# Optimization experiments

Hardware: AMD Instinct MI355X
Metric: run time of the kernel (lower is better)

## Reference

```python
import jax, jax.numpy as jnp
import numpy as np

B, S, D_IN, D_OUT, N, R = 8, 4096, 1280, 1280, 4, 16


def setup_inputs() -> dict:
    key = jax.random.key(0)
    ks = jax.random.split(key, 7)
    x = jax.random.normal(ks[0], (B, S, D_IN), dtype=jnp.float32)
    W = jax.random.normal(ks[1], (D_OUT, D_IN), dtype=jnp.float32) * 0.02
    bias = jax.random.normal(ks[2], (D_OUT,), dtype=jnp.float32) * 0.02
    A = jax.random.normal(ks[3], (N, R, D_IN), dtype=jnp.float32) * 0.02
    Bw = jax.random.normal(ks[4], (N, D_OUT, R), dtype=jnp.float32) * 0.02
    scalings = jax.random.uniform(ks[5], (N,), dtype=jnp.float32)
    masks = jax.random.uniform(ks[6], (N, S), dtype=jnp.float32)
    # normalize masks to sum ~1 per position, per docstring
    masks = masks / jnp.sum(masks, axis=0, keepdims=True)
    return {"x": x, "W": W, "bias": bias, "A": A, "Bw": Bw,
            "scalings": scalings, "masks": masks}


def reference(x, W, bias, A, Bw, scalings, masks):
    # base linear: y = x @ W^T + b
    base = jnp.einsum('bsd,od->bso', x, W) + bias
    # batched LoRA branches: h = x @ A_i^T  (b,s,n,r)
    h = jnp.einsum('bsd,nrd->bsnr', x, A)
    # lora_out_i = h @ B_i^T  (b,s,n,o)
    lora = jnp.einsum('bsnr,nor->bsno', h, Bw)
    # weighted sum over subjects: scaling_i * mask_i(pos)
    lora_sum = jnp.einsum('bsno,n,ns->bso', lora, scalings, masks)
    return base + lora_sum
```

## Files before the change

### kernel.cpp

```cpp
#include <hip/hip_runtime.h>
#include <hip/hip_bf16.h>
#include <stdint.h>

#define S_LEN   4096
#define DIN     1280
#define DOUT    1280
#define N_LORA  4
#define R_LORA  16
#define M_TOT   32768
#define KC      (DIN + N_LORA*R_LORA)

typedef __attribute__((ext_vector_type(4))) float floatx4;
typedef __attribute__((ext_vector_type(8))) short shortx8;

static __device__ __forceinline__ unsigned short bf16_rne(float f) {
    union { float f; unsigned u; } v; v.f = f;
    unsigned u = v.u;
    u += 0x7fffu + ((u >> 16) & 1u);
    return (unsigned short)(u >> 16);
}

static __device__ __forceinline__ void async16(const unsigned short* g, unsigned short* l) {
    __builtin_amdgcn_global_load_lds(
        (const __attribute__((address_space(1))) unsigned int*)g,
        (__attribute__((address_space(3))) unsigned int*)l, 16, 0, 0);
}

static __device__ __forceinline__ uint4 cvt8(const float* src) {
    const float4* p = (const float4*)src;
    float4 a = p[0], b = p[1];
    uint4 o;
    o.x = (unsigned)bf16_rne(a.x) | ((unsigned)bf16_rne(a.y) << 16);
    o.y = (unsigned)bf16_rne(a.z) | ((unsigned)bf16_rne(a.w) << 16);
    o.z = (unsigned)bf16_rne(b.x) | ((unsigned)bf16_rne(b.y) << 16);
    o.w = (unsigned)bf16_rne(b.z) | ((unsigned)bf16_rne(b.w) << 16);
    return o;
}

__global__ __launch_bounds__(256) void k_convert_x(const float* __restrict__ x,
                                                   unsigned short* __restrict__ xg) {
    int i = blockIdx.x * 256 + threadIdx.x;
    int e = i * 8;
    int m = e / DIN;
    int k = e - m * DIN;
    uint4 o = cvt8(x + e);
    *(uint4*)(xg + m * KC + k) = o;
}

__global__ __launch_bounds__(256) void k_build_wcat(const float* __restrict__ W,
                                                    const float* __restrict__ Bw,
                                                    unsigned short* __restrict__ Wcat) {
    int i = blockIdx.x * 256 + threadIdx.x;
    int e = i * 8;
    int o = e / KC;
    int c = e - o * KC;
    const float* src;
    if (c < DIN) {
        src = W + o * DIN + c;
    } else {
        int j = c - DIN;
        int n = j >> 4, r = j & 15;
        src = Bw + (n * DOUT + o) * R_LORA + r;
    }
    *(uint4*)(Wcat + o * KC + c) = cvt8(src);
}

__global__ __launch_bounds__(256) void k_convert_a(const float* __restrict__ A,
                                                   unsigned short* __restrict__ Ab) {
    int i = blockIdx.x * 256 + threadIdx.x;
    int e = i * 8;
    *(uint4*)(Ab + e) = cvt8(A + e);
}

__global__ __launch_bounds__(256) void k_lora_g(const unsigned short* __restrict__ xg_in,
                                                const unsigned short* __restrict__ Ab,
                                                const float* __restrict__ scalings,
                                                const float* __restrict__ masks,
                                                unsigned short* __restrict__ xg_out) {
    __shared__ unsigned short Xs[64 * 32];
    __shared__ unsigned short As[64 * 32];
    int tid = threadIdx.x;
    int wave = tid >> 6, lane = tid & 63;
    int mi = lane & 15, kq = lane >> 4;
    int m0 = blockIdx.x * 64;

    int chunk = tid;
    int srow = chunk >> 2;
    int skc  = (chunk & 3) * 8;

    floatx4 acc[4] = {};

    for (int k0 = 0; k0 < DIN; k0 += 32) {
        async16(xg_in + (m0 + srow) * KC + k0 + skc, Xs + chunk * 8);
        async16(Ab + srow * DIN + k0 + skc,          As + chunk * 8);
        __syncthreads();
        shortx8 xf = *(const shortx8*)(Xs + (wave * 16 + mi) * 32 + kq * 8);
#pragma unroll
        for (int ct = 0; ct < 4; ++ct) {
            shortx8 af = *(const shortx8*)(As + (ct * 16 + mi) * 32 + kq * 8);
            acc[ct] = __builtin_amdgcn_mfma_f32_16x16x32_bf16(xf, af, acc[ct], 0, 0, 0);
        }
        __syncthreads();
    }

#pragma unroll
    for (int ct = 0; ct < 4; ++ct) {
        float sc = scalings[ct];
        int j = ct * 16 + mi;
#pragma unroll
        for (int reg = 0; reg < 4; ++reg) {
            int m = m0 + wave * 16 + kq * 4 + reg;
            int s = m & (S_LEN - 1);
            float wgt = sc * masks[ct * S_LEN + s];
            xg_out[m * KC + DIN + j] = bf16_rne(acc[ct][reg] * wgt);
        }
    }
}

__global__ __launch_bounds__(256) void k_main_gemm(const unsigned short* __restrict__ xg,
                                                   const unsigned short* __restrict__ Wcat,
                                                   const float* __restrict__ bias,
                                                   float* __restrict__ out) {
    __shared__ unsigned short As[128 * 32];
    __shared__ unsigned short Bs[128 * 32];
    int tid = threadIdx.x;
    int wave = tid >> 6, lane = tid & 63;
    int bx = blockIdx.x;
    int cb = bx % 10, rb = bx / 10;
    int m0 = rb * 128, n0 = cb * 128;
    int wr = wave >> 1, wc = wave & 1;
    int mi = lane & 15, kq = lane >> 4;

    int c0 = tid, c1 = tid + 256;
    int ar0 = c0 >> 2, ak0 = (c0 & 3) * 8;
    int ar1 = c1 >> 2, ak1 = (c1 & 3) * 8;

    floatx4 acc[4][4] = {};

    for (int k0 = 0; k0 < KC; k0 += 32) {
        async16(xg   + (m0 + ar0) * KC + k0 + ak0, As + c0 * 8);
        async16(xg   + (m0 + ar1) * KC + k0 + ak1, As + c1 * 8);
        async16(Wcat + (n0 + ar0) * KC + k0 + ak0, Bs + c0 * 8);
        async16(Wcat + (n0 + ar1) * KC + k0 + ak1, Bs + c1 * 8);
        __syncthreads();
        shortx8 af[4], bf[4];
#pragma unroll
        for (int t = 0; t < 4; ++t) {
            af[t] = *(const shortx8*)(As + (wr * 64 + t * 16 + mi) * 32 + kq * 8);
            bf[t] = *(const shortx8*)(Bs + (wc * 64 + t * 16 + mi) * 32 + kq * 8);
        }
#pragma unroll
        for (int i = 0; i < 4; ++i)
#pragma unroll
            for (int j = 0; j < 4; ++j)
                acc[i][j] = __builtin_amdgcn_mfma_f32_16x16x32_bf16(af[i], bf[j], acc[i][j], 0, 0, 0);
        __syncthreads();
    }

#pragma unroll
    for (int j = 0; j < 4; ++j) {
        int col = n0 + wc * 64 + j * 16 + mi;
        float bv = bias[col];
#pragma unroll
        for (int i = 0; i < 4; ++i) {
            int rbase = m0 + wr * 64 + i * 16 + kq * 4;
#pragma unroll
            for (int reg = 0; reg < 4; ++reg) {
                out[(rbase + reg) * DOUT + col] = acc[i][j][reg] + bv;
            }
        }
    }
}

extern "C" void kernel_launch(void* const* d_in, const int* in_sizes, int n_in,
                              void* d_out, int out_size, void* d_ws, size_t ws_size,
                              hipStream_t stream) {
    const float* x     = (const float*)d_in[0];
    const float* W     = (const float*)d_in[1];
    const float* bias  = (const float*)d_in[2];
    const float* A     = (const float*)d_in[3];
    const float* Bw    = (const float*)d_in[4];
    const float* scal  = (const float*)d_in[5];
    const float* masks = (const float*)d_in[6];
    float* out = (float*)d_out;

    unsigned short* xg   = (unsigned short*)d_ws;
    unsigned short* Wcat = xg + (size_t)M_TOT * KC;
    unsigned short* Ab   = Wcat + (size_t)DOUT * KC;

    k_convert_x<<<(M_TOT * DIN) / (8 * 256), 256, 0, stream>>>(x, xg);
    k_build_wcat<<<(DOUT * KC) / (8 * 256), 256, 0, stream>>>(W, Bw, Wcat);
    k_convert_a<<<(N_LORA * R_LORA * DIN) / (8 * 256), 256, 0, stream>>>(A, Ab);
    k_lora_g<<<M_TOT / 64, 256, 0, stream>>>(xg, Ab, scal, masks, xg);
    k_main_gemm<<<(M_TOT / 128) * (DOUT / 128), 256, 0, stream>>>(xg, Wcat, bias, out);
}
```

Baseline: 470.7 us.

## Fuse x bf16 conversion into LoRA projection kernel and swizzle GEMM blocks per XCD

Removes the standalone x conversion kernel; the LoRA projection kernel now reads fp32 x directly, converts to bf16, stores it into the concatenated buffer and uses it as the MFMA operand from registers, avoiding an extra write/read round trip of x. The main GEMM block index is remapped so consecutive blocks on the same XCD cover contiguous row blocks for better L2 locality. A-weights are read directly from global memory without LDS staging, relying on cache hits.

Result: no change. 474.1 us (+0.7%).

```diff
diff --git a/kernel.cpp b/kernel.cpp
--- a/kernel.cpp
+++ b/kernel.cpp
@@ -12,6 +12,8 @@
 
 typedef __attribute__((ext_vector_type(4))) float floatx4;
 typedef __attribute__((ext_vector_type(8))) short shortx8;
+
+typedef union { uint4 u; shortx8 s; } punx8;
 
 static __device__ __forceinline__ unsigned short bf16_rne(float f) {
     union { float f; unsigned u; } v; v.f = f;
@@ -35,16 +37,6 @@
     o.z = (unsigned)bf16_rne(b.x) | ((unsigned)bf16_rne(b.y) << 16);
     o.w = (unsigned)bf16_rne(b.z) | ((unsigned)bf16_rne(b.w) << 16);
     return o;
-}
-
-__global__ __launch_bounds__(256) void k_convert_x(const float* __restrict__ x,
-                                                   unsigned short* __restrict__ xg) {
-    int i = blockIdx.x * 256 + threadIdx.x;
-    int e = i * 8;
-    int m = e / DIN;
-    int k = e - m * DIN;
-    uint4 o = cvt8(x + e);
-    *(uint4*)(xg + m * KC + k) = o;
 }
 
 __global__ __launch_bounds__(256) void k_build_wcat(const float* __restrict__ W,
@@ -72,35 +64,31 @@
     *(uint4*)(Ab + e) = cvt8(A + e);
 }
 
-__global__ __launch_bounds__(256) void k_lora_g(const unsigned short* __restrict__ xg_in,
-                                                const unsigned short* __restrict__ Ab,
-                                                const float* __restrict__ scalings,
-                                                const float* __restrict__ masks,
-                                                unsigned short* __restrict__ xg_out) {
-    __shared__ unsigned short Xs[64 * 32];
-    __shared__ unsigned short As[64 * 32];
+__global__ __launch_bounds__(256) void k_fused_x(const float* __restrict__ x,
+                                                 const unsigned short* __restrict__ Ab,
+                                                 const float* __restrict__ scalings,
+                                                 const float* __restrict__ masks,
+                                                 unsigned short* __restrict__ xg) {
     int tid = threadIdx.x;
     int wave = tid >> 6, lane = tid & 63;
     int mi = lane & 15, kq = lane >> 4;
     int m0 = blockIdx.x * 64;
+    int m = m0 + wave * 16 + mi;
 
-    int chunk = tid;
-    int srow = chunk >> 2;
-    int skc  = (chunk & 3) * 8;
+    const float* xrow = x + (size_t)m * DIN;
+    unsigned short* xgrow = xg + (size_t)m * KC;
 
     floatx4 acc[4] = {};
 
     for (int k0 = 0; k0 < DIN; k0 += 32) {
-        async16(xg_in + (m0 + srow) * KC + k0 + skc, Xs + chunk * 8);
-        async16(Ab + srow * DIN + k0 + skc,          As + chunk * 8);
-        __syncthreads();
-        shortx8 xf = *(const shortx8*)(Xs + (wave * 16 + mi) * 32 + kq * 8);
+        int k = k0 + kq * 8;
+        punx8 xf; xf.u = cvt8(xrow + k);
+        *(uint4*)(xgrow + k) = xf.u;
 #pragma unroll
         for (int ct = 0; ct < 4; ++ct) {
-            shortx8 af = *(const shortx8*)(As + (ct * 16 + mi) * 32 + kq * 8);
-            acc[ct] = __builtin_amdgcn_mfma_f32_16x16x32_bf16(xf, af, acc[ct], 0, 0, 0);
+            shortx8 bf = *(const shortx8*)(Ab + (ct * 16 + mi) * DIN + k);
+            acc[ct] = __builtin_amdgcn_mfma_f32_16x16x32_bf16(xf.s, bf, acc[ct], 0, 0, 0);
         }
-        __syncthreads();
     }
 
 #pragma unroll
@@ -109,10 +97,10 @@
         int j = ct * 16 + mi;
 #pragma unroll
         for (int reg = 0; reg < 4; ++reg) {
-            int m = m0 + wave * 16 + kq * 4 + reg;
-            int s = m & (S_LEN - 1);
+            int m2 = m0 + wave * 16 + kq * 4 + reg;
+            int s = m2 & (S_LEN - 1);
             float wgt = sc * masks[ct * S_LEN + s];
-            xg_out[m * KC + DIN + j] = bf16_rne(acc[ct][reg] * wgt);
+            xg[(size_t)m2 * KC + DIN + j] = bf16_rne(acc[ct][reg] * wgt);
         }
     }
 }
@@ -125,9 +113,14 @@
     __shared__ unsigned short Bs[128 * 32];
     int tid = threadIdx.x;
     int wave = tid >> 6, lane = tid & 63;
+
     int bx = blockIdx.x;
-    int cb = bx % 10, rb = bx / 10;
+    int xcd = bx & 7;
+    int slot = bx >> 3;
+    int rb = xcd * 32 + slot / 10;
+    int cb = slot % 10;
     int m0 = rb * 128, n0 = cb * 128;
+
     int wr = wave >> 1, wc = wave & 1;
     int mi = lane & 15, kq = lane >> 4;
 
@@ -166,7 +159,7 @@
             int rbase = m0 + wr * 64 + i * 16 + kq * 4;
 #pragma unroll
             for (int reg = 0; reg < 4; ++reg) {
-                out[(rbase + reg) * DOUT + col] = acc[i][j][reg] + bv;
+                out[(size_t)(rbase + reg) * DOUT + col] = acc[i][j][reg] + bv;
             }
         }
     }
@@ -188,9 +181,8 @@
     unsigned short* Wcat = xg + (size_t)M_TOT * KC;
     unsigned short* Ab   = Wcat + (size_t)DOUT * KC;
 
-    k_convert_x<<<(M_TOT * DIN) / (8 * 256), 256, 0, stream>>>(x, xg);
+    k_convert_a<<<(N_LORA * R_LORA * DIN) / (8 * 256), 256, 0, stream>>>(A, Ab);
     k_build_wcat<<<(DOUT * KC) / (8 * 256), 256, 0, stream>>>(W, Bw, Wcat);
-    k_convert_a<<<(N_LORA * R_LORA * DIN) / (8 * 256), 256, 0, stream>>>(A, Ab);
-    k_lora_g<<<M_TOT / 64, 256, 0, stream>>>(xg, Ab, scal, masks, xg);
+    k_fused_x<<<M_TOT / 64, 256, 0, stream>>>(x, Ab, scal, masks, xg);
     k_main_gemm<<<(M_TOT / 128) * (DOUT / 128), 256, 0, stream>>>(xg, Wcat, bias, out);
 }
```
